# Kernel optimization log

Hardware: AMD Instinct MI355X
Metric: run time of the kernel (lower is better)

Reference implementation:

```python
import jax, jax.numpy as jnp
import numpy as np

B, C, H, W = 4, 128, 64, 64
CQ = C // 8  # query/key channels = 16


def setup_inputs() -> dict:
    key = jax.random.key(0)
    ks = jax.random.split(key, 8)
    s = 0.05
    return {
        "x": jax.random.normal(ks[0], (B, C, H, W), jnp.float32),
        "wq": jax.random.normal(ks[1], (CQ, C), jnp.float32) * s,
        "bq": jax.random.normal(ks[2], (CQ,), jnp.float32) * s,
        "wk": jax.random.normal(ks[3], (CQ, C), jnp.float32) * s,
        "bk": jax.random.normal(ks[4], (CQ,), jnp.float32) * s,
        "wv": jax.random.normal(ks[5], (C, C), jnp.float32) * s,
        "bv": jax.random.normal(ks[6], (C,), jnp.float32) * s,
        # original inits gamma to 0; use small nonzero so attention path is exercised
        "gamma": jax.random.normal(ks[7], (1,), jnp.float32) * 0.1,
    }


def reference(x, wq, bq, wk, bk, wv, bv, gamma):
    b, c, h, w = x.shape
    n = h * w
    xf = x.reshape(b, c, n)  # [B, C, N]
    # 1x1 convs are per-position linear maps over channels
    q = jnp.einsum("qc,bcn->bnq", wq, xf) + bq            # [B, N, Cq]
    k = jnp.einsum("qc,bcn->bqn", wk, xf) + bk[:, None]   # [B, Cq, N]
    v = jnp.einsum("oc,bcn->bon", wv, xf) + bv[:, None]   # [B, C, N]
    # unscaled scores, softmax over keys (last dim), as in the original
    attn = jax.nn.softmax(jnp.einsum("bnq,bqm->bnm", q, k), axis=-1)  # [B, N, N]
    # out = value @ attention^T : out[b,c,n] = sum_m v[b,c,m] * attn[b,n,m]
    out = jnp.einsum("bom,bnm->bon", v, attn)             # [B, C, N]
    return gamma[0] * out.reshape(b, c, h, w) + x
```

## Files before the change

kernel.cpp:

```cpp
#include <hip/hip_runtime.h>
#include <hip/hip_bf16.h>

typedef float f32x4  __attribute__((ext_vector_type(4)));
typedef float f32x16 __attribute__((ext_vector_type(16)));
typedef short s16x8  __attribute__((ext_vector_type(8)));

#define NB 4
#define NC 128
#define NNPOS 4096
#define KSP 6
#define LOG2E 1.44269504088896f

__device__ __forceinline__ short bf16s(float x) {
    __hip_bfloat16 h = __float2bfloat16(x);
    return *reinterpret_cast<short*>(&h);
}
__device__ __forceinline__ int packbf2(float lo, float hi) {
    __hip_bfloat162 t = __float22bfloat162_rn(float2{lo, hi});
    return *reinterpret_cast<int*>(&t);
}
__device__ __forceinline__ float bf2f(unsigned short u) {
    unsigned int v = ((unsigned int)u) << 16;
    return *reinterpret_cast<float*>(&v);
}
__device__ __forceinline__ float exp2fast(float x) {
    return __builtin_amdgcn_exp2f(x);
}

__global__ __launch_bounds__(256) void qkv_kernel(
    const float* __restrict__ x,
    const float* __restrict__ wq, const float* __restrict__ bq,
    const float* __restrict__ wk, const float* __restrict__ bk,
    const float* __restrict__ wv, const float* __restrict__ bv,
    short* __restrict__ qb, short* __restrict__ kb, short* __restrict__ vt)
{
    const int n0  = blockIdx.x * 32;
    const int b   = blockIdx.y;
    const int tid = threadIdx.x;
    const int w = tid >> 6, lane = tid & 63, quad = lane >> 4, nn = lane & 15;

    __shared__ __align__(16) short xsT[32 * 136];
    __shared__ __align__(16) short vstage[4096];

    #pragma unroll
    for (int p = 0; p < 4; ++p) {
        int idx = tid + p * 256;
        int cc = idx >> 3, n4 = (idx & 7) * 4;
        f32x4 xv = *(const f32x4*)&x[((size_t)(b * NC + cc)) * NNPOS + n0 + n4];
        #pragma unroll
        for (int j = 0; j < 4; ++j)
            xsT[(n4 + j) * 136 + cc] = bf16s(xv[j]);
    }

    s16x8 af[3][4];
    bool  live[3];
    f32x4 biasv[3];
    #pragma unroll
    for (int t = 0; t < 3; ++t) {
        int rid = 3 * w + t;
        int R   = rid * 16;
        const float* wsrc = nullptr; const float* bsrc = nullptr; int row0 = 0;
        float scale = 1.0f;
        if (rid < 8)        { wsrc = wv; bsrc = bv; row0 = R; }
        else if (rid == 8)  { wsrc = wq; bsrc = bq; row0 = 0; scale = LOG2E; }
        else if (rid == 10) { wsrc = wk; bsrc = bk; row0 = 0; }
        live[t] = (wsrc != nullptr);
        #pragma unroll
        for (int r = 0; r < 4; ++r)
            biasv[t][r] = live[t] ? scale * bsrc[row0 + quad * 4 + r] : 0.0f;
        if (live[t]) {
            #pragma unroll
            for (int ks = 0; ks < 4; ++ks) {
                const float* src = wsrc + (size_t)(row0 + nn) * NC + ks * 32 + quad * 8;
                f32x4 wa = *(const f32x4*)src;
                f32x4 wb = *(const f32x4*)(src + 4);
                s16x8 f;
                #pragma unroll
                for (int j = 0; j < 4; ++j) {
                    f[j]     = bf16s(scale * wa[j]);
                    f[j + 4] = bf16s(scale * wb[j]);
                }
                af[t][ks] = f;
            }
        }
    }
    __syncthreads();

    f32x4 acc[3][2];
    #pragma unroll
    for (int t = 0; t < 3; ++t)
        #pragma unroll
        for (int nt = 0; nt < 2; ++nt)
            acc[t][nt] = biasv[t];

    #pragma unroll
    for (int nt = 0; nt < 2; ++nt) {
        s16x8 bf[4];
        #pragma unroll
        for (int ks = 0; ks < 4; ++ks)
            bf[ks] = *(const s16x8*)&xsT[(nt * 16 + nn) * 136 + ks * 32 + quad * 8];
        #pragma unroll
        for (int t = 0; t < 3; ++t)
            if (live[t])
                #pragma unroll
                for (int ks = 0; ks < 4; ++ks)
                    acc[t][nt] = __builtin_amdgcn_mfma_f32_16x16x32_bf16(af[t][ks], bf[ks], acc[t][nt], 0, 0, 0);
    }

    const int slot = (nn & 3) | ((nn & 4) << 1) | ((nn & 8) >> 1);

    #pragma unroll
    for (int t = 0; t < 3; ++t) {
        if (!live[t]) continue;
        const int rid = 3 * w + t;
        #pragma unroll
        for (int nt = 0; nt < 2; ++nt) {
            if (rid < 8) {
                #pragma unroll
                for (int r = 0; r < 4; ++r) {
                    int row = rid * 16 + quad * 4 + r;
                    vstage[(((nt << 2) | (row >> 5)) << 9) + ((row & 31) << 4) + slot]
                        = bf16s(acc[t][nt][r]);
                }
            } else {
                short4 pk;
                pk.x = bf16s(acc[t][nt][0]);
                pk.y = bf16s(acc[t][nt][1]);
                pk.z = bf16s(acc[t][nt][2]);
                pk.w = bf16s(acc[t][nt][3]);
                int n = n0 + nt * 16 + nn;
                short* dst = (rid == 8 ? qb : kb) +
                             ((size_t)(b * NNPOS) + n) * 16 + quad * 4;
                *reinterpret_cast<short4*>(dst) = pk;
            }
        }
    }
    __syncthreads();

    {
        short* vdst = vt + ((size_t)(b * 256) + (n0 >> 4)) * 2048;
        #pragma unroll
        for (int p = 0; p < 2; ++p) {
            int off = (tid + p * 256) * 8;
            *(s16x8*)&vdst[off] = *(const s16x8*)&vstage[off];
        }
    }
}

__global__ __launch_bounds__(256, 3) void attn_kernel(
    const short* __restrict__ qb, const short* __restrict__ kb,
    const short* __restrict__ vt,
    unsigned short* __restrict__ Ow, float* __restrict__ lw)
{
    const int s   = blockIdx.x;
    const int b   = blockIdx.z;
    const int tid = threadIdx.x;
    const int w = tid >> 6, lane = tid & 63, h = lane >> 5, c31 = lane & 31;

    const int q0 = (blockIdx.y * 4 + w) * 32;

    s16x8 bq = *(const s16x8*)(qb + ((size_t)(b * NNPOS) + q0 + c31) * 16 + h * 8);

    f32x16 acc[4];
    #pragma unroll
    for (int ct = 0; ct < 4; ++ct)
        #pragma unroll
        for (int r = 0; r < 16; ++r) acc[ct][r] = 0.0f;
    float lp0 = 0.f, lp1 = 0.f;

    const short* kbp = kb + (size_t)(b * NNPOS) * 16;
    const short* vbp = vt + (size_t)b * (256 * 4 * 512);
    const int nit    = (s < 4) ? 11 : 10;
    const int mbase  = (s < 4) ? s * 704 : 2816 + (s - 4) * 640;
    const int kgbase = mbase >> 4;
    const int voff = (c31 << 4) + (h << 3);

    f32x16 z;
    #pragma unroll
    for (int r = 0; r < 16; ++r) z[r] = 0.0f;

    int m0 = mbase;
    s16x8 ak0 = *(const s16x8*)(kbp + (size_t)(m0      + c31) * 16 + h * 8);
    s16x8 ak1 = *(const s16x8*)(kbp + (size_t)(m0 + 32 + c31) * 16 + h * 8);

    for (int it = 0; it < nit; ++it) {
        const int kg0 = kgbase + it * 4;

        s16x8 vb01[2][4];
        #pragma unroll
        for (int p = 0; p < 2; ++p)
            #pragma unroll
            for (int ct = 0; ct < 4; ++ct)
                vb01[p][ct] = *(const s16x8*)(vbp +
                    (((size_t)(kg0 + p) * 4 + ct) << 9) + voff);

        f32x16 s0 = __builtin_amdgcn_mfma_f32_32x32x16_bf16(ak0, bq, z, 0, 0, 0);
        f32x16 s1 = __builtin_amdgcn_mfma_f32_32x32x16_bf16(ak1, bq, z, 0, 0, 0);

        if (it + 1 < nit) {
            m0 += 64;
            ak0 = *(const s16x8*)(kbp + (size_t)(m0      + c31) * 16 + h * 8);
            ak1 = *(const s16x8*)(kbp + (size_t)(m0 + 32 + c31) * 16 + h * 8);
        }

        s16x8 pa[4];
        #pragma unroll
        for (int p = 0; p < 4; ++p) {
            const f32x16& sv = (p < 2) ? s0 : s1;
            const int off = (p & 1) * 8;
            union { int i[4]; s16x8 v; } u;
            #pragma unroll
            for (int j = 0; j < 4; ++j) {
                float p0 = exp2fast(sv[off + 2 * j]);
                float p1 = exp2fast(sv[off + 2 * j + 1]);
                if (j & 1) lp1 += p0 + p1; else lp0 += p0 + p1;
                u.i[j] = packbf2(p0, p1);
            }
            pa[p] = u.v;
        }

        __builtin_amdgcn_s_setprio(1);
        #pragma unroll
        for (int p = 0; p < 2; ++p)
            #pragma unroll
            for (int ct = 0; ct < 4; ++ct)
                acc[ct] = __builtin_amdgcn_mfma_f32_32x32x16_bf16(
                    pa[p], vb01[p][ct], acc[ct], 0, 0, 0);
        __builtin_amdgcn_s_setprio(0);

        s16x8 vb23[2][4];
        #pragma unroll
        for (int p = 0; p < 2; ++p)
            #pragma unroll
            for (int ct = 0; ct < 4; ++ct)
                vb23[p][ct] = *(const s16x8*)(vbp +
                    (((size_t)(kg0 + 2 + p) * 4 + ct) << 9) + voff);

        __builtin_amdgcn_s_setprio(1);
        #pragma unroll
        for (int p = 0; p < 2; ++p)
            #pragma unroll
            for (int ct = 0; ct < 4; ++ct)
                acc[ct] = __builtin_amdgcn_mfma_f32_32x32x16_bf16(
                    pa[2 + p], vb23[p][ct], acc[ct], 0, 0, 0);
        __builtin_amdgcn_s_setprio(0);
    }

    float lp = lp0 + lp1;
    lp += __shfl_xor(lp, 32, 64);
    if (lane < 32)
        lw[((size_t)(b * KSP + s)) * NNPOS + q0 + c31] = lp;

    #pragma unroll
    for (int ct = 0; ct < 4; ++ct)
        #pragma unroll
        for (int r = 0; r < 16; ++r) {
            int q = q0 + (r & 3) + 8 * (r >> 2) + 4 * h;
            Ow[(((size_t)(b * KSP + s)) * NNPOS + q) * NC + ct * 32 + c31] =
                (unsigned short)bf16s(acc[ct][r]);
        }
}

__global__ __launch_bounds__(256) void combine_kernel(
    const unsigned short* __restrict__ Ow, const float* __restrict__ lw,
    const float* __restrict__ x, const float* __restrict__ gamma,
    float* __restrict__ out)
{
    const int n0  = blockIdx.x * 64;
    const int b   = blockIdx.y;
    const int tid = threadIdx.x;

    __shared__ float ot[128 * 65 + 64];
    float* lsum = ot + 128 * 65;

    if (tid < 64) {
        float sl = 0.f;
        #pragma unroll
        for (int sI = 0; sI < KSP; ++sI)
            sl += lw[((size_t)(b * KSP + sI)) * NNPOS + n0 + tid];
        lsum[tid] = 1.0f / sl;
    }
    __syncthreads();

    #pragma unroll
    for (int p = 0; p < 4; ++p) {
        int e = tid + p * 256;
        int co = e & 15, n = e >> 4;
        float a[8] = {0.f, 0.f, 0.f, 0.f, 0.f, 0.f, 0.f, 0.f};
        #pragma unroll
        for (int sI = 0; sI < KSP; ++sI) {
            const unsigned short* src = Ow +
                (((size_t)(b * KSP + sI)) * NNPOS + n0 + n) * NC + co * 8;
            union { s16x8 v; unsigned short us[8]; } u;
            u.v = *(const s16x8*)src;
            #pragma unroll
            for (int j = 0; j < 8; ++j) a[j] += bf2f(u.us[j]);
        }
        float inv = lsum[n];
        #pragma unroll
        for (int j = 0; j < 8; ++j)
            ot[(co * 8 + j) * 65 + n] = a[j] * inv;
    }
    __syncthreads();

    const float g = gamma[0];
    #pragma unroll
    for (int p = 0; p < 8; ++p) {
        int e = tid + p * 256;
        int nq = e & 15, c = e >> 4;
        size_t a = ((size_t)(b * NC + c)) * NNPOS + n0 + nq * 4;
        float4 xv = *(const float4*)&x[a];
        float4 o;
        o.x = g * ot[c * 65 + nq * 4]     + xv.x;
        o.y = g * ot[c * 65 + nq * 4 + 1] + xv.y;
        o.z = g * ot[c * 65 + nq * 4 + 2] + xv.z;
        o.w = g * ot[c * 65 + nq * 4 + 3] + xv.w;
        *(float4*)&out[a] = o;
    }
}

extern "C" void kernel_launch(void* const* d_in, const int* in_sizes, int n_in,
                              void* d_out, int out_size, void* d_ws, size_t ws_size,
                              hipStream_t stream) {
    const float* x     = (const float*)d_in[0];
    const float* wq    = (const float*)d_in[1];
    const float* bq    = (const float*)d_in[2];
    const float* wk    = (const float*)d_in[3];
    const float* bk    = (const float*)d_in[4];
    const float* wv    = (const float*)d_in[5];
    const float* bv    = (const float*)d_in[6];
    const float* gamma = (const float*)d_in[7];
    float* out = (float*)d_out;

    short* qb = (short*)d_ws;
    short* kb = qb + (size_t)NB * NNPOS * 16;
    short* vt = kb + (size_t)NB * NNPOS * 16;
    unsigned short* Ow = (unsigned short*)(vt + (size_t)NB * NC * NNPOS);
    float* lw = (float*)(Ow + (size_t)NB * KSP * NNPOS * NC);

    qkv_kernel<<<dim3(128, NB), 256, 0, stream>>>(x, wq, bq, wk, bk, wv, bv, qb, kb, vt);
    attn_kernel<<<dim3(KSP, 32, NB), 256, 0, stream>>>(qb, kb, vt, Ow, lw);
    combine_kernel<<<dim3(NNPOS / 64, NB), 256, 0, stream>>>(Ow, lw, x, gamma, out);
}
```

Before: 119.8 us.

## Stage V tiles through double-buffered LDS via direct global-to-LDS loads

In the attention kernel, each wave used to load its own V fragments from global memory. Now the four waves of a block share a V tile that is copied straight into LDS with global_load_lds and double-buffered, so the next tile streams in while the current one is consumed. The qkv kernel's V staging layout is changed so each lane reads its fragment from LDS as one contiguous 16-byte load. This cuts redundant global/L2 traffic across waves, but adds a block-wide barrier every iteration, 32 KB of LDS per block that may limit occupancy, and drops the setprio hints.

New measurement: 114.3 us. 4.6% less time.

```diff
diff --git a/kernel.cpp b/kernel.cpp
--- a/kernel.cpp
+++ b/kernel.cpp
@@ -4,6 +4,7 @@
 typedef float f32x4  __attribute__((ext_vector_type(4)));
 typedef float f32x16 __attribute__((ext_vector_type(16)));
 typedef short s16x8  __attribute__((ext_vector_type(8)));
+typedef unsigned int u32;
 
 #define NB 4
 #define NC 128
@@ -25,6 +26,11 @@
 }
 __device__ __forceinline__ float exp2fast(float x) {
     return __builtin_amdgcn_exp2f(x);
+}
+__device__ __forceinline__ void gload_lds16(const short* g, short* l) {
+    __builtin_amdgcn_global_load_lds(
+        (const __attribute__((address_space(1))) u32*)g,
+        (__attribute__((address_space(3))) u32*)l, 16, 0, 0);
 }
 
 __global__ __launch_bounds__(256) void qkv_kernel(
@@ -119,7 +125,8 @@
                 #pragma unroll
                 for (int r = 0; r < 4; ++r) {
                     int row = rid * 16 + quad * 4 + r;
-                    vstage[(((nt << 2) | (row >> 5)) << 9) + ((row & 31) << 4) + slot]
+                    vstage[(((nt << 2) | (row >> 5)) << 9) +
+                           ((slot >> 3) << 8) + ((row & 31) << 3) + (slot & 7)]
                         = bf16s(acc[t][nt][r]);
                 }
             } else {
@@ -159,6 +166,8 @@
 
     const int q0 = (blockIdx.y * 4 + w) * 32;
 
+    __shared__ __align__(16) short vlds[2][8192];
+
     s16x8 bq = *(const s16x8*)(qb + ((size_t)(b * NNPOS) + q0 + c31) * 16 + h * 8);
 
     f32x16 acc[4];
@@ -169,30 +178,33 @@
     float lp0 = 0.f, lp1 = 0.f;
 
     const short* kbp = kb + (size_t)(b * NNPOS) * 16;
-    const short* vbp = vt + (size_t)b * (256 * 4 * 512);
     const int nit    = (s < 4) ? 11 : 10;
     const int mbase  = (s < 4) ? s * 704 : 2816 + (s - 4) * 640;
-    const int kgbase = mbase >> 4;
-    const int voff = (c31 << 4) + (h << 3);
+    const short* vtile = vt + (size_t)b * (NC * NNPOS) + ((size_t)(mbase >> 4) << 11);
 
     f32x16 z;
     #pragma unroll
     for (int r = 0; r < 16; ++r) z[r] = 0.0f;
 
+    #pragma unroll
+    for (int j = 0; j < 4; ++j)
+        gload_lds16(vtile + (tid << 3) + (j << 11),
+                    &vlds[0][0] + (tid << 3) + (j << 11));
     int m0 = mbase;
     s16x8 ak0 = *(const s16x8*)(kbp + (size_t)(m0      + c31) * 16 + h * 8);
     s16x8 ak1 = *(const s16x8*)(kbp + (size_t)(m0 + 32 + c31) * 16 + h * 8);
-
+    __syncthreads();
+
+    int buf = 0;
     for (int it = 0; it < nit; ++it) {
-        const int kg0 = kgbase + it * 4;
-
-        s16x8 vb01[2][4];
-        #pragma unroll
-        for (int p = 0; p < 2; ++p)
-            #pragma unroll
-            for (int ct = 0; ct < 4; ++ct)
-                vb01[p][ct] = *(const s16x8*)(vbp +
-                    (((size_t)(kg0 + p) * 4 + ct) << 9) + voff);
+        if (it + 1 < nit) {
+            const short* src = vtile + (((size_t)(it + 1)) << 13);
+            short* dst = &vlds[buf ^ 1][0];
+            #pragma unroll
+            for (int j = 0; j < 4; ++j)
+                gload_lds16(src + (tid << 3) + (j << 11),
+                            dst + (tid << 3) + (j << 11));
+        }
 
         f32x16 s0 = __builtin_amdgcn_mfma_f32_32x32x16_bf16(ak0, bq, z, 0, 0, 0);
         f32x16 s1 = __builtin_amdgcn_mfma_f32_32x32x16_bf16(ak1, bq, z, 0, 0, 0);
@@ -219,31 +231,18 @@
             pa[p] = u.v;
         }
 
-        __builtin_amdgcn_s_setprio(1);
-        #pragma unroll
-        for (int p = 0; p < 2; ++p)
-            #pragma unroll
-            for (int ct = 0; ct < 4; ++ct)
+        const short* vb = &vlds[buf][0];
+        #pragma unroll
+        for (int p = 0; p < 4; ++p)
+            #pragma unroll
+            for (int ct = 0; ct < 4; ++ct) {
+                s16x8 vf = *(const s16x8*)&vb[((p * 4 + ct) << 9) + (lane << 3)];
                 acc[ct] = __builtin_amdgcn_mfma_f32_32x32x16_bf16(
-                    pa[p], vb01[p][ct], acc[ct], 0, 0, 0);
-        __builtin_amdgcn_s_setprio(0);
-
-        s16x8 vb23[2][4];
-        #pragma unroll
-        for (int p = 0; p < 2; ++p)
-            #pragma unroll
-            for (int ct = 0; ct < 4; ++ct)
-                vb23[p][ct] = *(const s16x8*)(vbp +
-                    (((size_t)(kg0 + 2 + p) * 4 + ct) << 9) + voff);
-
-        __builtin_amdgcn_s_setprio(1);
-        #pragma unroll
-        for (int p = 0; p < 2; ++p)
-            #pragma unroll
-            for (int ct = 0; ct < 4; ++ct)
-                acc[ct] = __builtin_amdgcn_mfma_f32_32x32x16_bf16(
-                    pa[2 + p], vb23[p][ct], acc[ct], 0, 0, 0);
-        __builtin_amdgcn_s_setprio(0);
+                    pa[p], vf, acc[ct], 0, 0, 0);
+            }
+
+        __syncthreads();
+        buf ^= 1;
     }
 
     float lp = lp0 + lp1;
```

## Fuse split-K combine into attention kernel via in-block LDS reduction

Applied to the files above, without the earlier changes.

Each block now handles one 32-query tile, and its four waves each take a quarter of the keys. Partial outputs and row sums are reduced through shared memory, then normalized and added to the residual directly. This removes the separate combine kernel and the bf16 partial-output round trip through global memory. The V staging layout is changed so each lane reads a contiguous 16-byte chunk, and the setprio hints are dropped. The costs are fewer blocks (512 single-tile blocks at occupancy 2), a serial 16-iteration loop per wave, and LDS reduction overhead.

Result: faster. 111.1 us (-7.3%).

```diff
diff --git a/kernel.cpp b/kernel.cpp
--- a/kernel.cpp
+++ b/kernel.cpp
@@ -4,11 +4,11 @@
 typedef float f32x4  __attribute__((ext_vector_type(4)));
 typedef float f32x16 __attribute__((ext_vector_type(16)));
 typedef short s16x8  __attribute__((ext_vector_type(8)));
+typedef unsigned int u32;
 
 #define NB 4
 #define NC 128
 #define NNPOS 4096
-#define KSP 6
 #define LOG2E 1.44269504088896f
 
 __device__ __forceinline__ short bf16s(float x) {
@@ -19,12 +19,29 @@
     __hip_bfloat162 t = __float22bfloat162_rn(float2{lo, hi});
     return *reinterpret_cast<int*>(&t);
 }
-__device__ __forceinline__ float bf2f(unsigned short u) {
-    unsigned int v = ((unsigned int)u) << 16;
-    return *reinterpret_cast<float*>(&v);
-}
 __device__ __forceinline__ float exp2fast(float x) {
     return __builtin_amdgcn_exp2f(x);
+}
+
+__device__ __forceinline__ void exppack(const f32x16& sv, s16x8& plo, s16x8& phi,
+                                        float& l0, float& l1) {
+    union { int i[4]; s16x8 v; } u;
+    #pragma unroll
+    for (int j = 0; j < 4; ++j) {
+        float p0 = exp2fast(sv[2 * j]);
+        float p1 = exp2fast(sv[2 * j + 1]);
+        if (j & 1) l1 += p0 + p1; else l0 += p0 + p1;
+        u.i[j] = packbf2(p0, p1);
+    }
+    plo = u.v;
+    #pragma unroll
+    for (int j = 0; j < 4; ++j) {
+        float p0 = exp2fast(sv[8 + 2 * j]);
+        float p1 = exp2fast(sv[8 + 2 * j + 1]);
+        if (j & 1) l1 += p0 + p1; else l0 += p0 + p1;
+        u.i[j] = packbf2(p0, p1);
+    }
+    phi = u.v;
 }
 
 __global__ __launch_bounds__(256) void qkv_kernel(
@@ -119,7 +136,8 @@
                 #pragma unroll
                 for (int r = 0; r < 4; ++r) {
                     int row = rid * 16 + quad * 4 + r;
-                    vstage[(((nt << 2) | (row >> 5)) << 9) + ((row & 31) << 4) + slot]
+                    vstage[(((nt << 2) | (row >> 5)) << 9) +
+                           ((slot >> 3) << 8) + ((row & 31) << 3) + (slot & 7)]
                         = bf16s(acc[t][nt][r]);
                 }
             } else {
@@ -147,17 +165,23 @@
     }
 }
 
-__global__ __launch_bounds__(256, 3) void attn_kernel(
+__global__ __launch_bounds__(256, 2) void attn_kernel(
     const short* __restrict__ qb, const short* __restrict__ kb,
     const short* __restrict__ vt,
-    unsigned short* __restrict__ Ow, float* __restrict__ lw)
+    const float* __restrict__ xg, const float* __restrict__ gamma,
+    float* __restrict__ out)
 {
-    const int s   = blockIdx.x;
-    const int b   = blockIdx.z;
+    const int idx = blockIdx.x;
+    const int b   = (idx & 7) >> 1;
+    const int qy  = ((idx >> 3) << 1) | (idx & 1);
+    const int q0  = qy * 32;
     const int tid = threadIdx.x;
     const int w = tid >> 6, lane = tid & 63, h = lane >> 5, c31 = lane & 31;
 
-    const int q0 = (blockIdx.y * 4 + w) * 32;
+    __shared__ float cbufA[128][33];
+    __shared__ float cbufB[128][33];
+    __shared__ float lpbuf[4][32];
+    __shared__ float invbuf[32];
 
     s16x8 bq = *(const s16x8*)(qb + ((size_t)(b * NNPOS) + q0 + c31) * 16 + h * 8);
 
@@ -169,22 +193,19 @@
     float lp0 = 0.f, lp1 = 0.f;
 
     const short* kbp = kb + (size_t)(b * NNPOS) * 16;
-    const short* vbp = vt + (size_t)b * (256 * 4 * 512);
-    const int nit    = (s < 4) ? 11 : 10;
-    const int mbase  = (s < 4) ? s * 704 : 2816 + (s - 4) * 640;
-    const int kgbase = mbase >> 4;
-    const int voff = (c31 << 4) + (h << 3);
+    const short* vbp = vt + (size_t)b * (NC * NNPOS);
 
     f32x16 z;
     #pragma unroll
     for (int r = 0; r < 16; ++r) z[r] = 0.0f;
 
-    int m0 = mbase;
+    int m0 = w * 1024;
     s16x8 ak0 = *(const s16x8*)(kbp + (size_t)(m0      + c31) * 16 + h * 8);
     s16x8 ak1 = *(const s16x8*)(kbp + (size_t)(m0 + 32 + c31) * 16 + h * 8);
 
-    for (int it = 0; it < nit; ++it) {
-        const int kg0 = kgbase + it * 4;
+    #pragma unroll 1
+    for (int it = 0; it < 16; ++it) {
+        const int kg0 = (w * 1024 >> 4) + it * 4;
 
         s16x8 vb01[2][4];
         #pragma unroll
@@ -192,41 +213,28 @@
             #pragma unroll
             for (int ct = 0; ct < 4; ++ct)
                 vb01[p][ct] = *(const s16x8*)(vbp +
-                    (((size_t)(kg0 + p) * 4 + ct) << 9) + voff);
-
-        f32x16 s0 = __builtin_amdgcn_mfma_f32_32x32x16_bf16(ak0, bq, z, 0, 0, 0);
-        f32x16 s1 = __builtin_amdgcn_mfma_f32_32x32x16_bf16(ak1, bq, z, 0, 0, 0);
-
-        if (it + 1 < nit) {
+                    (((size_t)(kg0 + p) * 4 + ct) << 9) + (lane << 3));
+
+        s16x8 pa[4];
+        {
+            f32x16 sc = __builtin_amdgcn_mfma_f32_32x32x16_bf16(ak0, bq, z, 0, 0, 0);
+            exppack(sc, pa[0], pa[1], lp0, lp1);
+            sc = __builtin_amdgcn_mfma_f32_32x32x16_bf16(ak1, bq, z, 0, 0, 0);
+            exppack(sc, pa[2], pa[3], lp0, lp1);
+        }
+
+        if (it + 1 < 16) {
             m0 += 64;
             ak0 = *(const s16x8*)(kbp + (size_t)(m0      + c31) * 16 + h * 8);
             ak1 = *(const s16x8*)(kbp + (size_t)(m0 + 32 + c31) * 16 + h * 8);
         }
 
-        s16x8 pa[4];
-        #pragma unroll
-        for (int p = 0; p < 4; ++p) {
-            const f32x16& sv = (p < 2) ? s0 : s1;
-            const int off = (p & 1) * 8;
-            union { int i[4]; s16x8 v; } u;
-            #pragma unroll
-            for (int j = 0; j < 4; ++j) {
-                float p0 = exp2fast(sv[off + 2 * j]);
-                float p1 = exp2fast(sv[off + 2 * j + 1]);
-                if (j & 1) lp1 += p0 + p1; else lp0 += p0 + p1;
-                u.i[j] = packbf2(p0, p1);
-            }
-            pa[p] = u.v;
-        }
-
-        __builtin_amdgcn_s_setprio(1);
         #pragma unroll
         for (int p = 0; p < 2; ++p)
             #pragma unroll
             for (int ct = 0; ct < 4; ++ct)
                 acc[ct] = __builtin_amdgcn_mfma_f32_32x32x16_bf16(
                     pa[p], vb01[p][ct], acc[ct], 0, 0, 0);
-        __builtin_amdgcn_s_setprio(0);
 
         s16x8 vb23[2][4];
         #pragma unroll
@@ -234,88 +242,62 @@
             #pragma unroll
             for (int ct = 0; ct < 4; ++ct)
                 vb23[p][ct] = *(const s16x8*)(vbp +
-                    (((size_t)(kg0 + 2 + p) * 4 + ct) << 9) + voff);
-
-        __builtin_amdgcn_s_setprio(1);
+                    (((size_t)(kg0 + 2 + p) * 4 + ct) << 9) + (lane << 3));
         #pragma unroll
         for (int p = 0; p < 2; ++p)
             #pragma unroll
             for (int ct = 0; ct < 4; ++ct)
                 acc[ct] = __builtin_amdgcn_mfma_f32_32x32x16_bf16(
                     pa[2 + p], vb23[p][ct], acc[ct], 0, 0, 0);
-        __builtin_amdgcn_s_setprio(0);
     }
 
     float lp = lp0 + lp1;
     lp += __shfl_xor(lp, 32, 64);
-    if (lane < 32)
-        lw[((size_t)(b * KSP + s)) * NNPOS + q0 + c31] = lp;
-
-    #pragma unroll
-    for (int ct = 0; ct < 4; ++ct)
-        #pragma unroll
-        for (int r = 0; r < 16; ++r) {
-            int q = q0 + (r & 3) + 8 * (r >> 2) + 4 * h;
-            Ow[(((size_t)(b * KSP + s)) * NNPOS + q) * NC + ct * 32 + c31] =
-                (unsigned short)bf16s(acc[ct][r]);
-        }
-}
-
-__global__ __launch_bounds__(256) void combine_kernel(
-    const unsigned short* __restrict__ Ow, const float* __restrict__ lw,
-    const float* __restrict__ x, const float* __restrict__ gamma,
-    float* __restrict__ out)
-{
-    const int n0  = blockIdx.x * 64;
-    const int b   = blockIdx.y;
-    const int tid = threadIdx.x;
-
-    __shared__ float ot[128 * 65 + 64];
-    float* lsum = ot + 128 * 65;
-
-    if (tid < 64) {
-        float sl = 0.f;
-        #pragma unroll
-        for (int sI = 0; sI < KSP; ++sI)
-            sl += lw[((size_t)(b * KSP + sI)) * NNPOS + n0 + tid];
-        lsum[tid] = 1.0f / sl;
+    if (lane < 32) lpbuf[w][c31] = lp;
+
+    if (w < 2) {
+        float (*cb)[33] = (w == 0) ? cbufA : cbufB;
+        #pragma unroll
+        for (int ct = 0; ct < 4; ++ct)
+            #pragma unroll
+            for (int r = 0; r < 16; ++r) {
+                int q = (r & 3) + 8 * (r >> 2) + 4 * h;
+                cb[ct * 32 + c31][q] = acc[ct][r];
+            }
     }
     __syncthreads();
 
-    #pragma unroll
-    for (int p = 0; p < 4; ++p) {
-        int e = tid + p * 256;
-        int co = e & 15, n = e >> 4;
-        float a[8] = {0.f, 0.f, 0.f, 0.f, 0.f, 0.f, 0.f, 0.f};
-        #pragma unroll
-        for (int sI = 0; sI < KSP; ++sI) {
-            const unsigned short* src = Ow +
-                (((size_t)(b * KSP + sI)) * NNPOS + n0 + n) * NC + co * 8;
-            union { s16x8 v; unsigned short us[8]; } u;
-            u.v = *(const s16x8*)src;
-            #pragma unroll
-            for (int j = 0; j < 8; ++j) a[j] += bf2f(u.us[j]);
-        }
-        float inv = lsum[n];
-        #pragma unroll
-        for (int j = 0; j < 8; ++j)
-            ot[(co * 8 + j) * 65 + n] = a[j] * inv;
-    }
+    if (w >= 2) {
+        float (*cb)[33] = (w == 2) ? cbufA : cbufB;
+        #pragma unroll
+        for (int ct = 0; ct < 4; ++ct)
+            #pragma unroll
+            for (int r = 0; r < 16; ++r) {
+                int q = (r & 3) + 8 * (r >> 2) + 4 * h;
+                cb[ct * 32 + c31][q] += acc[ct][r];
+            }
+    }
+    if (tid < 32)
+        invbuf[tid] = 1.0f / (lpbuf[0][tid] + lpbuf[1][tid] +
+                              lpbuf[2][tid] + lpbuf[3][tid]);
     __syncthreads();
 
-    const float g = gamma[0];
-    #pragma unroll
-    for (int p = 0; p < 8; ++p) {
-        int e = tid + p * 256;
-        int nq = e & 15, c = e >> 4;
-        size_t a = ((size_t)(b * NC + c)) * NNPOS + n0 + nq * 4;
-        float4 xv = *(const float4*)&x[a];
-        float4 o;
-        o.x = g * ot[c * 65 + nq * 4]     + xv.x;
-        o.y = g * ot[c * 65 + nq * 4 + 1] + xv.y;
-        o.z = g * ot[c * 65 + nq * 4 + 2] + xv.z;
-        o.w = g * ot[c * 65 + nq * 4 + 3] + xv.w;
-        *(float4*)&out[a] = o;
+    {
+        const float g = gamma[0];
+        const int c  = tid >> 1;
+        const int nh = (tid & 1) * 16;
+        size_t base = ((size_t)(b * NC + c)) * NNPOS + q0 + nh;
+        #pragma unroll
+        for (int j = 0; j < 16; j += 4) {
+            f32x4 xv = *(const f32x4*)&xg[base + j];
+            f32x4 o;
+            #pragma unroll
+            for (int e = 0; e < 4; ++e) {
+                int q = nh + j + e;
+                o[e] = g * (cbufA[c][q] + cbufB[c][q]) * invbuf[q] + xv[e];
+            }
+            *(f32x4*)&out[base + j] = o;
+        }
     }
 }
 
@@ -335,10 +317,7 @@
     short* qb = (short*)d_ws;
     short* kb = qb + (size_t)NB * NNPOS * 16;
     short* vt = kb + (size_t)NB * NNPOS * 16;
-    unsigned short* Ow = (unsigned short*)(vt + (size_t)NB * NC * NNPOS);
-    float* lw = (float*)(Ow + (size_t)NB * KSP * NNPOS * NC);
 
     qkv_kernel<<<dim3(128, NB), 256, 0, stream>>>(x, wq, bq, wk, bk, wv, bv, qb, kb, vt);
-    attn_kernel<<<dim3(KSP, 32, NB), 256, 0, stream>>>(qb, kb, vt, Ow, lw);
-    combine_kernel<<<dim3(NNPOS / 64, NB), 256, 0, stream>>>(Ow, lw, x, gamma, out);
-}
+    attn_kernel<<<dim3(512), 256, 0, stream>>>(qb, kb, vt, x, gamma, out);
+}
```
